# Performance work log

Measured on AMD Instinct MI355X. Metric: run time of the kernel, lower is better.

The kernel has to match this reference:

```python
import jax, jax.numpy as jnp
import numpy as np

N_SRC, N_DST, N_EDGES, E = 100000, 50000, 600000, 128

def setup_inputs() -> dict:
    key = jax.random.key(0)
    k1, k2, k3, k4, k5, k6 = jax.random.split(key, 6)
    return {
        "h_src": jax.random.normal(k1, (N_SRC, E), dtype=jnp.float32),
        "weights": jax.random.uniform(k2, (N_EDGES,), dtype=jnp.float32),
        "src_idx": jax.random.randint(k3, (N_EDGES,), 0, N_SRC, dtype=jnp.int32),
        "dst_idx": jax.random.randint(k4, (N_EDGES,), 0, N_DST, dtype=jnp.int32),
        "num_dst": N_DST,
        "q_w": jax.random.normal(k5, (E, E), dtype=jnp.float32) * (2.0 / np.sqrt(E + E)),  # xavier-ish, gain=sqrt(2)
        "q_b": jnp.zeros((E,), dtype=jnp.float32),
        "w_w": jax.random.normal(k6, (E, 2 * E), dtype=jnp.float32) * (2.0 / np.sqrt(E + 2 * E)),
        "w_b": jnp.zeros((E,), dtype=jnp.float32),
    }

def reference(h_src, weights, src_idx, dst_idx, num_dst, q_w, q_b, w_w, w_b):
    h_dst = h_src[:num_dst]                                  # [n_dst, E]
    n = jax.nn.relu(h_src @ q_w.T + q_b)                     # [n_src, E] (dropout=eval/no-op)
    w = weights.astype(jnp.float32)
    m = n[src_idx] * w[:, None]                              # [n_edges, E] edge messages
    agg = jax.ops.segment_sum(m, dst_idx, num_segments=num_dst)   # weighted feature sum
    ws = jax.ops.segment_sum(w, dst_idx, num_segments=num_dst)    # weight sum
    ws = jnp.clip(ws, 1.0, None)[:, None]                    # clamp(min=1)
    z = jnp.concatenate([h_dst, agg / ws], axis=1)           # [n_dst, 2E]
    z = jax.nn.relu(z @ w_w.T + w_b)                         # [n_dst, E]
    z_norm = jnp.linalg.norm(z, axis=1, keepdims=True)
    z_norm = jnp.where(z_norm == 0, 1.0, z_norm)
    return z / z_norm
```

## Files before the change

### kernel.cpp

```cpp
#include <hip/hip_runtime.h>
#include <math.h>


typedef __attribute__((ext_vector_type(8))) short  short8;
typedef __attribute__((ext_vector_type(8))) __bf16 bf16x8;
typedef __attribute__((ext_vector_type(4))) float  f32x4;

#define MFMA16(a, b, c) __builtin_amdgcn_mfma_f32_16x16x32_bf16( \
    __builtin_bit_cast(bf16x8, (a)), __builtin_bit_cast(bf16x8, (b)), (c), 0, 0, 0)

#define EDGE_CAP 4096

__device__ __forceinline__ ushort f2bf(float x) {
    unsigned u = __float_as_uint(x);
    return (ushort)((u + 0x7fffu + ((u >> 16) & 1u)) >> 16);
}
__device__ __forceinline__ float bfhi(unsigned p) { return __uint_as_float(p & 0xffff0000u); }
__device__ __forceinline__ float bflo(unsigned p) { return __uint_as_float(p << 16); }

__device__ __forceinline__ short8 cvt8(float4 v0, float4 v1) {
    ushort t[8] = { f2bf(v0.x), f2bf(v0.y), f2bf(v0.z), f2bf(v0.w),
                    f2bf(v1.x), f2bf(v1.y), f2bf(v1.z), f2bf(v1.w) };
    return *(short8*)t;
}

__global__ __launch_bounds__(512) void k_gemm1_hist(const float* __restrict__ h,
    const float* __restrict__ qw, const float* __restrict__ qb,
    ushort* __restrict__ nout, int nrows, int t1,
    const int* __restrict__ dst, int* __restrict__ hist, int nedges, int nb)
{
    __shared__ __align__(16) ushort aL[128 * 128];
    __shared__ __align__(16) ushort bL[128 * 128];
    const int tid = threadIdx.x;

    if (blockIdx.x >= t1) {
        int* hl = (int*)aL;
        const int g = blockIdx.x - t1;
        const int G = gridDim.x - t1;
        for (int i = tid; i < nb; i += 512) hl[i] = 0;
        __syncthreads();
        const int chunk = (nedges + G - 1) / G;
        const int e0 = g * chunk, e1 = min(e0 + chunk, nedges);
        for (int e = e0 + tid; e < e1; e += 512)
            atomicAdd(&hl[dst[e] >> 6], 1);
        __syncthreads();
        for (int i = tid; i < nb; i += 512) hist[i * G + g] = hl[i];
        return;
    }

    const int rb = blockIdx.x * 128;
    const int rr = tid >> 4, sl = tid & 15;

    #pragma unroll
    for (int rg = 0; rg < 4; ++rg) {
        int row = rg * 32 + rr, gr = rb + row;
        float4 a0 = make_float4(0.f,0.f,0.f,0.f), a1 = a0;
        if (gr < nrows) {
            a0 = *(const float4*)&h[(size_t)gr * 128 + sl * 8];
            a1 = *(const float4*)&h[(size_t)gr * 128 + sl * 8 + 4];
        }
        *(short8*)&aL[row * 128 + (sl ^ (row & 7)) * 8] = cvt8(a0, a1);
        float4 b0 = *(const float4*)&qw[row * 128 + sl * 8];
        float4 b1 = *(const float4*)&qw[row * 128 + sl * 8 + 4];
        *(short8*)&bL[row * 128 + (sl ^ (row & 7)) * 8] = cvt8(b0, b1);
    }
    __syncthreads();

    const int w = tid >> 6, l = tid & 63;
    const int lr = l & 15, lk = l >> 4;
    const int row = w * 16 + lr;

    short8 a[4];
    #pragma unroll
    for (int ks = 0; ks < 4; ++ks)
        a[ks] = *(const short8*)&aL[row * 128 + ((ks * 4 + lk) ^ (lr & 7)) * 8];

    f32x4 acc[8];
    #pragma unroll
    for (int nt = 0; nt < 8; ++nt) acc[nt] = (f32x4){0.f, 0.f, 0.f, 0.f};

    #pragma unroll
    for (int nt = 0; nt < 8; ++nt)
        #pragma unroll
        for (int ks = 0; ks < 4; ++ks) {
            short8 b = *(const short8*)&bL[(nt * 16 + lr) * 128 + ((ks * 4 + lk) ^ (lr & 7)) * 8];
            acc[nt] = MFMA16(b, a[ks], acc[nt]);
        }

    const int gr = rb + row;
    if (gr < nrows) {
        #pragma unroll
        for (int nt = 0; nt < 8; ++nt) {
            float4 bv = *(const float4*)&qb[nt * 16 + lk * 4];
            ushort t[4];
            t[0] = f2bf(fmaxf(acc[nt][0] + bv.x, 0.f));
            t[1] = f2bf(fmaxf(acc[nt][1] + bv.y, 0.f));
            t[2] = f2bf(fmaxf(acc[nt][2] + bv.z, 0.f));
            t[3] = f2bf(fmaxf(acc[nt][3] + bv.w, 0.f));
            *(ushort4*)&nout[(size_t)gr * 128 + nt * 16 + lk * 4] = *(ushort4*)t;
        }
    }
}

__global__ __launch_bounds__(1024) void k_scan_blk(const int* __restrict__ counts,
    int* __restrict__ offs, int* __restrict__ partials, int n)
{
    __shared__ int wtot[16];
    const int tid = threadIdx.x, lane = tid & 63, wv = tid >> 6;
    const int idx = blockIdx.x * 1024 + tid;
    int v = (idx < n) ? counts[idx] : 0;
    int x = v;
    #pragma unroll
    for (int off = 1; off < 64; off <<= 1) {
        int y = __shfl_up(x, off);
        if (lane >= off) x += y;
    }
    if (lane == 63) wtot[wv] = x;
    __syncthreads();
    if (tid == 0) {
        int r = 0;
        #pragma unroll
        for (int q = 0; q < 16; ++q) { int t = wtot[q]; wtot[q] = r; r += t; }
    }
    __syncthreads();
    if (idx < n) offs[idx] = wtot[wv] + x - v;
    if (tid == 1023) partials[blockIdx.x] = wtot[15] + x;
}

__global__ void k_scan_part(int* __restrict__ partials, int nb)
{
    __shared__ int wsum2[2];
    const int tid = threadIdx.x, lane = tid & 63, wv = tid >> 6;
    int v = (tid < nb) ? partials[tid] : 0;
    int x = v;
    #pragma unroll
    for (int off = 1; off < 64; off <<= 1) {
        int y = __shfl_up(x, off);
        if (lane >= off) x += y;
    }
    if (lane == 63) wsum2[wv] = x;
    __syncthreads();
    int add = (wv == 1) ? wsum2[0] : 0;
    if (tid < nb) partials[tid] = add + x - v;
}

__global__ __launch_bounds__(256) void k_part(const int* __restrict__ src,
    const int* __restrict__ dst, const float* __restrict__ w,
    const int* __restrict__ binoff0, const int* __restrict__ parts,
    int2* __restrict__ eb, int nedges, int nb)
{
    __shared__ int cur[1024];
    const int g = blockIdx.x, tid = threadIdx.x, G = gridDim.x;
    for (int b = tid; b < nb; b += 256) {
        int i = b * G + g;
        cur[b] = binoff0[i] + parts[i >> 10];
    }
    __syncthreads();
    const int chunk = (nedges + G - 1) / G;
    const int e0 = g * chunk, e1 = min(e0 + chunk, nedges);
    for (int e = e0 + tid; e < e1; e += 256) {
        int d = dst[e];
        int pos = atomicAdd(&cur[d >> 6], 1);
        eb[pos] = make_int2(((d & 63) << 17) | src[e], __float_as_int(w[e]));
    }
}

__global__ __launch_bounds__(256) void k_bsort_gather(const ushort* __restrict__ nsrc,
    const int2* __restrict__ eb, const int* __restrict__ binoff0,
    const int* __restrict__ parts, ushort* __restrict__ z2,
    int ndst, int nedges, int G, int NB)
{
    __shared__ int2 els[EDGE_CAP];
    __shared__ int  base[65];
    __shared__ int  cur[64];
    const int b = blockIdx.x, tid = threadIdx.x;
    const int i0 = b * G;
    const int j0 = binoff0[i0] + parts[i0 >> 10];
    int j1 = nedges;
    if (b != NB - 1) {
        int i1 = (b + 1) * G;
        j1 = binoff0[i1] + parts[i1 >> 10];
    }
    const int cnt_e = j1 - j0;

    if (tid < 64) cur[tid] = 0;
    __syncthreads();
    for (int j = j0 + tid; j < j1; j += 256)
        atomicAdd(&cur[eb[j].x >> 17], 1);
    __syncthreads();

    if (tid < 64) {
        int a = cur[tid];
        int x = a;
        #pragma unroll
        for (int off = 1; off < 64; off <<= 1) {
            int y = __shfl_up(x, off);
            if (tid >= off) x += y;
        }
        base[tid] = x - a;
        cur[tid]  = x - a;
        if (tid == 63) base[64] = x;
    }
    __syncthreads();

    const int wv = tid >> 6, lane = tid & 63;
    const int g = lane >> 4, s = lane & 15;

    if (cnt_e <= EDGE_CAP) {
        for (int j = j0 + tid; j < j1; j += 256) {
            int2 e = eb[j];
            int pos = atomicAdd(&cur[e.x >> 17], 1);
            els[pos] = make_int2(e.x & 0x1FFFF, e.y);
        }
        __syncthreads();

        for (int r = wv; r < 64; r += 4) {
            int gr = b * 64 + r;
            if (gr >= ndst) break;
            const int ja = base[r], jb = base[r + 1];
            float acc[8] = {0.f,0.f,0.f,0.f,0.f,0.f,0.f,0.f};
            float ws = 0.f;
            for (int j = ja + g; j < jb; j += 4) {
                int2 ew = els[j];
                float we = __int_as_float(ew.y);
                short8 rv = *(const short8*)&nsrc[(size_t)ew.x * 128 + s * 8];
                uint4 p = __builtin_bit_cast(uint4, rv);
                acc[0] = fmaf(bflo(p.x), we, acc[0]);
                acc[1] = fmaf(bfhi(p.x), we, acc[1]);
                acc[2] = fmaf(bflo(p.y), we, acc[2]);
                acc[3] = fmaf(bfhi(p.y), we, acc[3]);
                acc[4] = fmaf(bflo(p.z), we, acc[4]);
                acc[5] = fmaf(bfhi(p.z), we, acc[5]);
                acc[6] = fmaf(bflo(p.w), we, acc[6]);
                acc[7] = fmaf(bfhi(p.w), we, acc[7]);
                ws += we;
            }
            #pragma unroll
            for (int i = 0; i < 8; ++i) {
                acc[i] += __shfl_xor(acc[i], 16);
                acc[i] += __shfl_xor(acc[i], 32);
            }
            ws += __shfl_xor(ws, 16);
            ws += __shfl_xor(ws, 32);
            if (g == 0) {
                float inv = 1.f / fmaxf(ws, 1.f);
                ushort t8[8];
                #pragma unroll
                for (int i = 0; i < 8; ++i) t8[i] = f2bf(acc[i] * inv);
                *(short8*)&z2[(size_t)gr * 128 + s * 8] = *(short8*)t8;
            }
        }
    } else {
        for (int r = wv; r < 64; r += 4) {
            int gr = b * 64 + r;
            if (gr >= ndst) break;
            float acc[8] = {0.f,0.f,0.f,0.f,0.f,0.f,0.f,0.f};
            float ws = 0.f;
            for (int j = j0 + g; j < j1; j += 4) {
                int2 e = eb[j];
                if ((e.x >> 17) != r) continue;
                float we = __int_as_float(e.y);
                short8 rv = *(const short8*)&nsrc[(size_t)(e.x & 0x1FFFF) * 128 + s * 8];
                uint4 p = __builtin_bit_cast(uint4, rv);
                acc[0] = fmaf(bflo(p.x), we, acc[0]);
                acc[1] = fmaf(bfhi(p.x), we, acc[1]);
                acc[2] = fmaf(bflo(p.y), we, acc[2]);
                acc[3] = fmaf(bfhi(p.y), we, acc[3]);
                acc[4] = fmaf(bflo(p.z), we, acc[4]);
                acc[5] = fmaf(bfhi(p.z), we, acc[5]);
                acc[6] = fmaf(bflo(p.w), we, acc[6]);
                acc[7] = fmaf(bfhi(p.w), we, acc[7]);
                ws += we;
            }
            #pragma unroll
            for (int i = 0; i < 8; ++i) {
                acc[i] += __shfl_xor(acc[i], 16);
                acc[i] += __shfl_xor(acc[i], 32);
            }
            ws += __shfl_xor(ws, 16);
            ws += __shfl_xor(ws, 32);
            if (g == 0) {
                float inv = 1.f / fmaxf(ws, 1.f);
                ushort t8[8];
                #pragma unroll
                for (int i = 0; i < 8; ++i) t8[i] = f2bf(acc[i] * inv);
                *(short8*)&z2[(size_t)gr * 128 + s * 8] = *(short8*)t8;
            }
        }
    }
}

__global__ __launch_bounds__(512) void k_gemm2(const float* __restrict__ h,
    const ushort* __restrict__ z2, const float* __restrict__ ww,
    const float* __restrict__ wb, float* __restrict__ out, int nrows)
{
    __shared__ __align__(16) ushort aL[128 * 128];
    __shared__ __align__(16) ushort bL[128 * 128];
    const int tid = threadIdx.x;
    const int rb  = blockIdx.x * 128;
    const int rr = tid >> 4, sl = tid & 15;

    const int w = tid >> 6, l = tid & 63;
    const int lr = l & 15, lk = l >> 4;
    const int row = w * 16 + lr;

    f32x4 acc[8];
    #pragma unroll
    for (int nt = 0; nt < 8; ++nt) acc[nt] = (f32x4){0.f, 0.f, 0.f, 0.f};

    #pragma unroll
    for (int ph = 0; ph < 2; ++ph) {
        if (ph) __syncthreads();
        #pragma unroll
        for (int rg = 0; rg < 4; ++rg) {
            int r2 = rg * 32 + rr, gr = rb + r2;
            short8 av = (short8){0,0,0,0,0,0,0,0};
            if (gr < nrows) {
                if (ph == 0) {
                    float4 a0 = *(const float4*)&h[(size_t)gr * 128 + sl * 8];
                    float4 a1 = *(const float4*)&h[(size_t)gr * 128 + sl * 8 + 4];
                    av = cvt8(a0, a1);
                } else {
                    av = *(const short8*)&z2[(size_t)gr * 128 + sl * 8];
                }
            }
            *(short8*)&aL[r2 * 128 + (sl ^ (r2 & 7)) * 8] = av;
            float4 b0 = *(const float4*)&ww[r2 * 256 + ph * 128 + sl * 8];
            float4 b1 = *(const float4*)&ww[r2 * 256 + ph * 128 + sl * 8 + 4];
            *(short8*)&bL[r2 * 128 + (sl ^ (r2 & 7)) * 8] = cvt8(b0, b1);
        }
        __syncthreads();

        short8 a[4];
        #pragma unroll
        for (int ks = 0; ks < 4; ++ks)
            a[ks] = *(const short8*)&aL[row * 128 + ((ks * 4 + lk) ^ (lr & 7)) * 8];

        #pragma unroll
        for (int nt = 0; nt < 8; ++nt)
            #pragma unroll
            for (int ks = 0; ks < 4; ++ks) {
                short8 b = *(const short8*)&bL[(nt * 16 + lr) * 128 + ((ks * 4 + lk) ^ (lr & 7)) * 8];
                acc[nt] = MFMA16(b, a[ks], acc[nt]);
            }
    }

    float val[8][4];
    float ss = 0.f;
    #pragma unroll
    for (int nt = 0; nt < 8; ++nt) {
        float4 bv = *(const float4*)&wb[nt * 16 + lk * 4];
        #pragma unroll
        for (int v = 0; v < 4; ++v) {
            float x = acc[nt][v] + ((const float*)&bv)[v];
            x = fmaxf(x, 0.f);
            val[nt][v] = x;
            ss = fmaf(x, x, ss);
        }
    }
    ss += __shfl_xor(ss, 16);
    ss += __shfl_xor(ss, 32);
    float nr = sqrtf(ss);
    nr = (nr == 0.f) ? 1.f : nr;
    float inv = 1.f / nr;

    const int gr = rb + row;
    if (gr < nrows) {
        #pragma unroll
        for (int nt = 0; nt < 8; ++nt) {
            float4 o;
            o.x = val[nt][0] * inv; o.y = val[nt][1] * inv;
            o.z = val[nt][2] * inv; o.w = val[nt][3] * inv;
            *(float4*)&out[(size_t)gr * 128 + nt * 16 + lk * 4] = o;
        }
    }
}

extern "C" void kernel_launch(void* const* d_in, const int* in_sizes, int n_in,
                              void* d_out, int out_size, void* d_ws, size_t ws_size,
                              hipStream_t stream)
{
    const float* h   = (const float*)d_in[0];
    const float* wts = (const float*)d_in[1];
    const int*   src = (const int*)d_in[2];
    const int*   dst = (const int*)d_in[3];
    const float* qw  = (const float*)d_in[5];
    const float* qb  = (const float*)d_in[6];
    const float* www = (const float*)d_in[7];
    const float* wb  = (const float*)d_in[8];
    float* out = (float*)d_out;

    const int n_src   = in_sizes[0] / 128;
    const int n_edges = in_sizes[1];
    const int n_dst   = out_size / 128;

    const int G  = 128;
    const int NB = (n_dst + 63) / 64;
    const int NBINS = NB * G;

    ushort* nbuf    = (ushort*)d_ws;
    ushort* z2      = nbuf + (size_t)n_src * 128;
    int2*   eb      = (int2*)(z2 + (size_t)n_dst * 128);
    int*    hist    = (int*)(eb + n_edges);
    int*    binoff0 = hist + NBINS;
    int*    parts   = binoff0 + NBINS;

    const int t1 = (n_src + 127) / 128;
    k_gemm1_hist<<<t1 + G, 512, 0, stream>>>(h, qw, qb, nbuf, n_src, t1,
                                             dst, hist, n_edges, NB);

    const int nbs = (NBINS + 1023) / 1024;
    k_scan_blk<<<nbs, 1024, 0, stream>>>(hist, binoff0, parts, NBINS);
    k_scan_part<<<1, 128, 0, stream>>>(parts, nbs);

    k_part<<<G, 256, 0, stream>>>(src, dst, wts, binoff0, parts, eb, n_edges, NB);

    k_bsort_gather<<<NB, 256, 0, stream>>>(nbuf, eb, binoff0, parts, z2,
                                           n_dst, n_edges, G, NB);

    const int t2 = (n_dst + 127) / 128;
    k_gemm2<<<t2, 512, 0, stream>>>(h, z2, www, wb, out, n_dst);
}
```

Measured before the change: 100.3 us.

## Fuse gather-aggregate with second GEMM and merge scan kernels via last-block ticket

The per-bin gather/normalize kernel now keeps its 64-row aggregated features in shared memory and runs the second GEMM, ReLU and L2 normalization directly. This removes the z2 round trip through global memory and one launch. The two-stage prefix scan is merged into one kernel in which the last block to finish, chosen by an atomic ticket, scans the partials. This removes another launch. In exchange, every 64-row block must reload and convert the full 128x256 weight matrix, and the GEMM runs with 256-thread blocks instead of 512.

```diff
diff --git a/kernel.cpp b/kernel.cpp
--- a/kernel.cpp
+++ b/kernel.cpp
@@ -27,7 +27,8 @@
 __global__ __launch_bounds__(512) void k_gemm1_hist(const float* __restrict__ h,
     const float* __restrict__ qw, const float* __restrict__ qb,
     ushort* __restrict__ nout, int nrows, int t1,
-    const int* __restrict__ dst, int* __restrict__ hist, int nedges, int nb)
+    const int* __restrict__ dst, int* __restrict__ hist, int nedges, int nb,
+    int* __restrict__ done)
 {
     __shared__ __align__(16) ushort aL[128 * 128];
     __shared__ __align__(16) ushort bL[128 * 128];
@@ -37,6 +38,7 @@
         int* hl = (int*)aL;
         const int g = blockIdx.x - t1;
         const int G = gridDim.x - t1;
+        if (g == 0 && tid == 0) *done = 0;
         for (int i = tid; i < nb; i += 512) hl[i] = 0;
         __syncthreads();
         const int chunk = (nedges + G - 1) / G;
@@ -102,10 +104,12 @@
     }
 }
 
-__global__ __launch_bounds__(1024) void k_scan_blk(const int* __restrict__ counts,
-    int* __restrict__ offs, int* __restrict__ partials, int n)
+__global__ __launch_bounds__(1024) void k_scan(const int* __restrict__ counts,
+    int* __restrict__ offs, int* __restrict__ partials, int* __restrict__ done,
+    int n, int nbs)
 {
     __shared__ int wtot[16];
+    __shared__ int ticket;
     const int tid = threadIdx.x, lane = tid & 63, wv = tid >> 6;
     const int idx = blockIdx.x * 1024 + tid;
     int v = (idx < n) ? counts[idx] : 0;
@@ -125,23 +129,29 @@
     __syncthreads();
     if (idx < n) offs[idx] = wtot[wv] + x - v;
     if (tid == 1023) partials[blockIdx.x] = wtot[15] + x;
-}
-
-__global__ void k_scan_part(int* __restrict__ partials, int nb)
-{
-    __shared__ int wsum2[2];
-    const int tid = threadIdx.x, lane = tid & 63, wv = tid >> 6;
-    int v = (tid < nb) ? partials[tid] : 0;
-    int x = v;
-    #pragma unroll
-    for (int off = 1; off < 64; off <<= 1) {
-        int y = __shfl_up(x, off);
-        if (lane >= off) x += y;
-    }
-    if (lane == 63) wsum2[wv] = x;
-    __syncthreads();
-    int add = (wv == 1) ? wsum2[0] : 0;
-    if (tid < nb) partials[tid] = add + x - v;
+
+    __threadfence();
+    if (tid == 0) ticket = atomicAdd(done, 1);
+    __syncthreads();
+    if (ticket == nbs - 1) {
+        __threadfence();
+        int v2 = (tid < nbs) ? partials[tid] : 0;
+        int x2 = v2;
+        #pragma unroll
+        for (int off = 1; off < 64; off <<= 1) {
+            int y = __shfl_up(x2, off);
+            if (lane >= off) x2 += y;
+        }
+        if (lane == 63) wtot[wv] = x2;
+        __syncthreads();
+        if (tid == 0) {
+            int r = 0;
+            #pragma unroll
+            for (int q = 0; q < 16; ++q) { int t = wtot[q]; wtot[q] = r; r += t; }
+        }
+        __syncthreads();
+        if (tid < nbs) partials[tid] = wtot[wv] + x2 - v2;
+    }
 }
 
 __global__ __launch_bounds__(256) void k_part(const int* __restrict__ src,
@@ -165,15 +175,33 @@
     }
 }
 
-__global__ __launch_bounds__(256) void k_bsort_gather(const ushort* __restrict__ nsrc,
-    const int2* __restrict__ eb, const int* __restrict__ binoff0,
-    const int* __restrict__ parts, ushort* __restrict__ z2,
-    int ndst, int nedges, int G, int NB)
+__global__ __launch_bounds__(256) void k_gather_gemm2(const float* __restrict__ h,
+    const ushort* __restrict__ nsrc, const int2* __restrict__ eb,
+    const int* __restrict__ binoff0, const int* __restrict__ parts,
+    const float* __restrict__ ww, const float* __restrict__ wb,
+    float* __restrict__ out, int ndst, int nedges, int G, int NB)
 {
-    __shared__ int2 els[EDGE_CAP];
-    __shared__ int  base[65];
-    __shared__ int  cur[64];
+    __shared__ __align__(16) char ubuf[EDGE_CAP * 8];
+    __shared__ __align__(16) ushort z2L[64 * 128];
+    __shared__ __align__(16) ushort hA[64 * 128];
+    __shared__ int cnt[64];
+    __shared__ int base[65];
+    int2*   els = (int2*)ubuf;
+    ushort* bB  = (ushort*)ubuf;
+
     const int b = blockIdx.x, tid = threadIdx.x;
+
+    for (int f = tid; f < 64 * 16; f += 256) {
+        int r = f >> 4, sl = f & 15;
+        int gr = b * 64 + r;
+        float4 a0 = make_float4(0.f,0.f,0.f,0.f), a1 = a0;
+        if (gr < ndst) {
+            a0 = *(const float4*)&h[(size_t)gr * 128 + sl * 8];
+            a1 = *(const float4*)&h[(size_t)gr * 128 + sl * 8 + 4];
+        }
+        *(short8*)&hA[r * 128 + (sl ^ (r & 7)) * 8] = cvt8(a0, a1);
+    }
+
     const int i0 = b * G;
     const int j0 = binoff0[i0] + parts[i0 >> 10];
     int j1 = nedges;
@@ -183,14 +211,14 @@
     }
     const int cnt_e = j1 - j0;
 
-    if (tid < 64) cur[tid] = 0;
+    if (tid < 64) cnt[tid] = 0;
     __syncthreads();
     for (int j = j0 + tid; j < j1; j += 256)
-        atomicAdd(&cur[eb[j].x >> 17], 1);
+        atomicAdd(&cnt[eb[j].x >> 17], 1);
     __syncthreads();
 
     if (tid < 64) {
-        int a = cur[tid];
+        int a = cnt[tid];
         int x = a;
         #pragma unroll
         for (int off = 1; off < 64; off <<= 1) {
@@ -198,7 +226,7 @@
             if (tid >= off) x += y;
         }
         base[tid] = x - a;
-        cur[tid]  = x - a;
+        cnt[tid]  = x - a;
         if (tid == 63) base[64] = x;
     }
     __syncthreads();
@@ -209,14 +237,12 @@
     if (cnt_e <= EDGE_CAP) {
         for (int j = j0 + tid; j < j1; j += 256) {
             int2 e = eb[j];
-            int pos = atomicAdd(&cur[e.x >> 17], 1);
+            int pos = atomicAdd(&cnt[e.x >> 17], 1);
             els[pos] = make_int2(e.x & 0x1FFFF, e.y);
         }
         __syncthreads();
 
         for (int r = wv; r < 64; r += 4) {
-            int gr = b * 64 + r;
-            if (gr >= ndst) break;
             const int ja = base[r], jb = base[r + 1];
             float acc[8] = {0.f,0.f,0.f,0.f,0.f,0.f,0.f,0.f};
             float ws = 0.f;
@@ -247,13 +273,11 @@
                 ushort t8[8];
                 #pragma unroll
                 for (int i = 0; i < 8; ++i) t8[i] = f2bf(acc[i] * inv);
-                *(short8*)&z2[(size_t)gr * 128 + s * 8] = *(short8*)t8;
+                *(short8*)&z2L[r * 128 + (s ^ (r & 7)) * 8] = *(short8*)t8;
             }
         }
     } else {
         for (int r = wv; r < 64; r += 4) {
-            int gr = b * 64 + r;
-            if (gr >= ndst) break;
             float acc[8] = {0.f,0.f,0.f,0.f,0.f,0.f,0.f,0.f};
             float ws = 0.f;
             for (int j = j0 + g; j < j1; j += 4) {
@@ -284,64 +308,42 @@
                 ushort t8[8];
                 #pragma unroll
                 for (int i = 0; i < 8; ++i) t8[i] = f2bf(acc[i] * inv);
-                *(short8*)&z2[(size_t)gr * 128 + s * 8] = *(short8*)t8;
-            }
-        }
-    }
-}
-
-__global__ __launch_bounds__(512) void k_gemm2(const float* __restrict__ h,
-    const ushort* __restrict__ z2, const float* __restrict__ ww,
-    const float* __restrict__ wb, float* __restrict__ out, int nrows)
-{
-    __shared__ __align__(16) ushort aL[128 * 128];
-    __shared__ __align__(16) ushort bL[128 * 128];
-    const int tid = threadIdx.x;
-    const int rb  = blockIdx.x * 128;
-    const int rr = tid >> 4, sl = tid & 15;
-
-    const int w = tid >> 6, l = tid & 63;
-    const int lr = l & 15, lk = l >> 4;
-    const int row = w * 16 + lr;
-
-    f32x4 acc[8];
-    #pragma unroll
-    for (int nt = 0; nt < 8; ++nt) acc[nt] = (f32x4){0.f, 0.f, 0.f, 0.f};
+                *(short8*)&z2L[r * 128 + (s ^ (r & 7)) * 8] = *(short8*)t8;
+            }
+        }
+    }
+    __syncthreads();
+
+    const int lr = lane & 15, lk = lane >> 4;
+    const int rowloc = wv * 16 + lr;
+
+    f32x4 acc2[8];
+    #pragma unroll
+    for (int nt = 0; nt < 8; ++nt) acc2[nt] = (f32x4){0.f, 0.f, 0.f, 0.f};
 
     #pragma unroll
     for (int ph = 0; ph < 2; ++ph) {
         if (ph) __syncthreads();
-        #pragma unroll
-        for (int rg = 0; rg < 4; ++rg) {
-            int r2 = rg * 32 + rr, gr = rb + r2;
-            short8 av = (short8){0,0,0,0,0,0,0,0};
-            if (gr < nrows) {
-                if (ph == 0) {
-                    float4 a0 = *(const float4*)&h[(size_t)gr * 128 + sl * 8];
-                    float4 a1 = *(const float4*)&h[(size_t)gr * 128 + sl * 8 + 4];
-                    av = cvt8(a0, a1);
-                } else {
-                    av = *(const short8*)&z2[(size_t)gr * 128 + sl * 8];
-                }
-            }
-            *(short8*)&aL[r2 * 128 + (sl ^ (r2 & 7)) * 8] = av;
-            float4 b0 = *(const float4*)&ww[r2 * 256 + ph * 128 + sl * 8];
-            float4 b1 = *(const float4*)&ww[r2 * 256 + ph * 128 + sl * 8 + 4];
-            *(short8*)&bL[r2 * 128 + (sl ^ (r2 & 7)) * 8] = cvt8(b0, b1);
-        }
-        __syncthreads();
-
+        for (int f = tid; f < 128 * 16; f += 256) {
+            int col = f >> 4, sl2 = f & 15;
+            float4 b0 = *(const float4*)&ww[col * 256 + ph * 128 + sl2 * 8];
+            float4 b1 = *(const float4*)&ww[col * 256 + ph * 128 + sl2 * 8 + 4];
+            *(short8*)&bB[col * 128 + (sl2 ^ (col & 7)) * 8] = cvt8(b0, b1);
+        }
+        __syncthreads();
+
+        const ushort* A = ph ? z2L : hA;
         short8 a[4];
         #pragma unroll
         for (int ks = 0; ks < 4; ++ks)
-            a[ks] = *(const short8*)&aL[row * 128 + ((ks * 4 + lk) ^ (lr & 7)) * 8];
+            a[ks] = *(const short8*)&A[rowloc * 128 + ((ks * 4 + lk) ^ (lr & 7)) * 8];
 
         #pragma unroll
         for (int nt = 0; nt < 8; ++nt)
             #pragma unroll
             for (int ks = 0; ks < 4; ++ks) {
-                short8 b = *(const short8*)&bL[(nt * 16 + lr) * 128 + ((ks * 4 + lk) ^ (lr & 7)) * 8];
-                acc[nt] = MFMA16(b, a[ks], acc[nt]);
+                short8 bb = *(const short8*)&bB[(nt * 16 + lr) * 128 + ((ks * 4 + lk) ^ (lr & 7)) * 8];
+                acc2[nt] = MFMA16(bb, a[ks], acc2[nt]);
             }
     }
 
@@ -352,7 +354,7 @@
         float4 bv = *(const float4*)&wb[nt * 16 + lk * 4];
         #pragma unroll
         for (int v = 0; v < 4; ++v) {
-            float x = acc[nt][v] + ((const float*)&bv)[v];
+            float x = acc2[nt][v] + ((const float*)&bv)[v];
             x = fmaxf(x, 0.f);
             val[nt][v] = x;
             ss = fmaf(x, x, ss);
@@ -364,8 +366,8 @@
     nr = (nr == 0.f) ? 1.f : nr;
     float inv = 1.f / nr;
 
-    const int gr = rb + row;
-    if (gr < nrows) {
+    const int gr = b * 64 + rowloc;
+    if (gr < ndst) {
         #pragma unroll
         for (int nt = 0; nt < 8; ++nt) {
             float4 o;
@@ -399,25 +401,21 @@
     const int NBINS = NB * G;
 
     ushort* nbuf    = (ushort*)d_ws;
-    ushort* z2      = nbuf + (size_t)n_src * 128;
-    int2*   eb      = (int2*)(z2 + (size_t)n_dst * 128);
+    int2*   eb      = (int2*)(nbuf + (size_t)n_src * 128);
     int*    hist    = (int*)(eb + n_edges);
     int*    binoff0 = hist + NBINS;
     int*    parts   = binoff0 + NBINS;
+    int*    done    = parts + 128;
 
     const int t1 = (n_src + 127) / 128;
     k_gemm1_hist<<<t1 + G, 512, 0, stream>>>(h, qw, qb, nbuf, n_src, t1,
-                                             dst, hist, n_edges, NB);
+                                             dst, hist, n_edges, NB, done);
 
     const int nbs = (NBINS + 1023) / 1024;
-    k_scan_blk<<<nbs, 1024, 0, stream>>>(hist, binoff0, parts, NBINS);
-    k_scan_part<<<1, 128, 0, stream>>>(parts, nbs);
+    k_scan<<<nbs, 1024, 0, stream>>>(hist, binoff0, parts, done, NBINS, nbs);
 
     k_part<<<G, 256, 0, stream>>>(src, dst, wts, binoff0, parts, eb, n_edges, NB);
 
-    k_bsort_gather<<<NB, 256, 0, stream>>>(nbuf, eb, binoff0, parts, z2,
-                                           n_dst, n_edges, G, NB);
-
-    const int t2 = (n_dst + 127) / 128;
-    k_gemm2<<<t2, 512, 0, stream>>>(h, z2, www, wb, out, n_dst);
-}
+    k_gather_gemm2<<<NB, 256, 0, stream>>>(h, nbuf, eb, binoff0, parts,
+                                           www, wb, out, n_dst, n_edges, G, NB);
+}
```

Result: slower. 152.9 us (+52.5%).
